# Optimization experiments

Measured on AMD Instinct MI355X. Metric: run time of the kernel, lower is better.

## Reference

```python
import jax, jax.numpy as jnp
from jax import lax
import numpy as np

B, L1, L2 = 64, 1024, 1024


def setup_inputs() -> dict:
    key = jax.random.key(0)
    ks = jax.random.split(key, 6)
    s1 = 1.0 / np.sqrt(L1)
    s2 = 1.0 / np.sqrt(L2)
    return {
        "a": jax.random.normal(ks[0], (B, L1), dtype=jnp.float32),
        "b": jax.random.normal(ks[1], (B, L2), dtype=jnp.float32),
        # nn.Linear(L1, L1) and nn.Linear(L2, L2) params (PyTorch default uniform init range)
        "W1": jax.random.uniform(ks[2], (L1, L1), jnp.float32, -s1, s1),
        "b1": jax.random.uniform(ks[3], (L1,), jnp.float32, -s1, s1),
        "W2": jax.random.uniform(ks[4], (L2, L2), jnp.float32, -s2, s2),
        "b2": jax.random.uniform(ks[5], (L2,), jnp.float32, -s2, s2),
    }


def _dtw_cost(cost):
    """DTW accumulated-cost DP for one [N, M] pairwise-cost matrix.

    R[i,j] = cost[i,j] + min(R[i-1,j-1], R[i-1,j], R[i,j-1]).
    The within-row dependency x[j] = c[j] + min(m[j], x[j-1]) is a min-plus
    prefix: x[j] = S[j] + cummin(m - S_{j-1}) with S = cumsum(c), which lets
    each row be computed in parallel (wavefront-equivalent vectorization).
    Returns the scalar DTW distance R[N-1, M-1].
    """
    dt = cost.dtype
    row0 = jnp.cumsum(cost[0])  # R[0, :]

    def step(prev_row, c_row):
        # m[j] = min(R[i-1, j], R[i-1, j-1]);  j=0 has no (i-1, j-1) neighbor
        shifted = jnp.concatenate([jnp.full((1,), jnp.inf, dt), prev_row[:-1]])
        m = jnp.minimum(prev_row, shifted)
        S = jnp.cumsum(c_row)
        S_prev = jnp.concatenate([jnp.zeros((1,), dt), S[:-1]])
        row = S + lax.associative_scan(jnp.minimum, m - S_prev)
        return row, None

    last_row, _ = lax.scan(step, row0, cost[1:])
    return last_row[-1]


def reference(a, b, W1, b1, W2, b2):
    # seq1 / seq2 linear projections over the time axis
    a_p = a @ W1.T + b1  # [B, L1]
    b_p = b @ W2.T + b2  # [B, L2]
    # squared-euclidean pairwise cost (scipy.sqeuclidean on scalar elements)
    cost = (a_p[:, :, None] - b_p[:, None, :]) ** 2  # [B, L1, L2]
    return jax.vmap(_dtw_cost)(cost)  # [B] DTW distances
```

## Files before the change

kernel.cpp:

```cpp
#include <hip/hip_runtime.h>
#include <math.h>


#define L 1024
#define BATCH 64

__global__ __launch_bounds__(256) void proj_kernel(
    const float* __restrict__ a, const float* __restrict__ b,
    const float* __restrict__ W1, const float* __restrict__ b1,
    const float* __restrict__ W2, const float* __restrict__ b2,
    float* __restrict__ ap, float* __restrict__ bp, int KC) {
  int part = blockIdx.x >> 7;
  int sub = blockIdx.x & 127;
  const float* X;
  const float* W;
  const float* bias;
  float* out;
  int i0;
  if (sub < 64) {
    X = a; W = W1; bias = b1; out = ap + part * BATCH * L; i0 = sub * 16;
  } else {
    X = b; W = W2; bias = b2; out = bp + part * BATCH * L; i0 = (sub - 64) * 16;
  }

  __shared__ float a_s[64][36];
  __shared__ float w_s[16][36];

  int tid = threadIdx.x;
  int lane_b = tid & 63;
  int iq = tid >> 6;

  float acc[4] = {0.f, 0.f, 0.f, 0.f};

  int kbeg = part * KC;
  int kend = kbeg + KC;
  for (int k0 = kbeg; k0 < kend; k0 += 32) {
    {
      int row = tid >> 2;
      int kl = (tid & 3) * 8;
      const float4* src = reinterpret_cast<const float4*>(&X[row * L + k0 + kl]);
      float4 v0 = src[0];
      float4 v1 = src[1];
      *reinterpret_cast<float4*>(&a_s[row][kl]) = v0;
      *reinterpret_cast<float4*>(&a_s[row][kl + 4]) = v1;
    }
    {
      int row = tid >> 4;
      int kl = (tid & 15) * 2;
      float2 v = *reinterpret_cast<const float2*>(&W[(i0 + row) * L + k0 + kl]);
      w_s[row][kl] = v.x;
      w_s[row][kl + 1] = v.y;
    }
    __syncthreads();
    #pragma unroll
    for (int kl = 0; kl < 32; kl += 4) {
      float4 av = *reinterpret_cast<const float4*>(&a_s[lane_b][kl]);
      #pragma unroll
      for (int m = 0; m < 4; ++m) {
        float4 wv = *reinterpret_cast<const float4*>(&w_s[iq * 4 + m][kl]);
        acc[m] += av.x * wv.x + av.y * wv.y + av.z * wv.z + av.w * wv.w;
      }
    }
    __syncthreads();
  }

  #pragma unroll
  for (int m = 0; m < 4; ++m) {
    int i = i0 + iq * 4 + m;
    float bv = (part == 0) ? bias[i] : 0.f;
    out[lane_b * L + i] = acc[m] + bv;
  }
}


#define NW 4
#define CPL 4
#define KBAR 32
#define OFF 31
#define NG 67
#define APOFF 864
#define APPAD 3048

__device__ __forceinline__ float dpp_shr1_z(float v) {
  int r = __builtin_amdgcn_update_dpp(0, __float_as_int(v), 0x138, 0xf, 0xf,
                                      true);
  return __int_as_float(r);
}

__device__ __forceinline__ float dpp_shl1_z(float v) {
  int r = __builtin_amdgcn_update_dpp(0, __float_as_int(v), 0x130, 0xf, 0xf,
                                      true);
  return __int_as_float(r);
}

__device__ __forceinline__ float min3f(float x, float y, float z) {
  float r;
  asm("v_min3_f32 %0, %1, %2, %3" : "=v"(r) : "v"(x), "v"(y), "v"(z));
  return r;
}

__global__ __launch_bounds__(256, 1) void dtw_kernel(
    const float* __restrict__ app, const float* __restrict__ bpp,
    float* __restrict__ out, int parts) {
  const int b = blockIdx.x;
  const int tid = threadIdx.x;
  const int w = tid >> 6;
  const int t = tid & 63;
  const int woff = OFF * w;
  const float INF = INFINITY;

  __shared__ float ap_pad[APPAD];
  __shared__ float ring[NW - 1][64];

  for (int idx = tid; idx < APPAD; idx += 256) {
    int src = idx - APOFF;
    float v = INF;
    if ((unsigned)src < (unsigned)L) {
      v = app[b * L + src];
      for (int p = 1; p < parts; ++p) v += app[p * BATCH * L + b * L + src];
    }
    ap_pad[idx] = v;
  }
  if (tid < (NW - 1) * 64) reinterpret_cast<float*>(ring)[tid] = INF;

  const int colb = tid * CPL;
  float4 bv = *reinterpret_cast<const float4*>(&bpp[b * L + colb]);
  for (int p = 1; p < parts; ++p) {
    float4 u = *reinterpret_cast<const float4*>(
        &bpp[p * BATCH * L + b * L + colb]);
    bv.x += u.x; bv.y += u.y; bv.z += u.z; bv.w += u.w;
  }
  const float bpv0 = bv.x, bpv1 = bv.y, bpv2 = bv.z, bpv3 = bv.w;

  float p1_0 = INF, p1_1 = INF, p1_2 = INF, p1_3 = INF;
  float p2_0 = INF, p2_1 = INF, p2_2 = INF, p2_3 = INF;
  float A0 = INF, A1 = INF, A2 = INF, A3 = INF;
  float ringchunk = INF, feedprev = INF, vprod = INF, apchunk;
  float res = 0.f;
  const bool lane0 = (t == 0);
  const bool lane63 = (t == 63);
  const int apbase = APOFF + t - (256 + OFF) * w;

  __syncthreads();

#define DTW_GROUP(s0v, FIRSTG, LASTG)                                        \
  {                                                                          \
    const int s0 = (s0v);                                                    \
    apchunk = ap_pad[apbase + s0];                                           \
    if (w == 0)                                                              \
      ringchunk = INF;                                                       \
    else if (t < KBAR)                                                       \
      ringchunk = ring[w - 1][(s0 + t - woff - 1) & 63];                     \
    _Pragma("unroll")                                                        \
    for (int k = 0; k < KBAR; ++k) {                                         \
      float sh1 = dpp_shr1_z(p1_3);                                          \
      float sh2 = dpp_shr1_z(p2_3);                                          \
      float sha = dpp_shr1_z(A3);                                            \
      float p1m1 = lane0 ? ringchunk : sh1;                                  \
      float p2m1 = lane0 ? feedprev : sh2;                                   \
      if ((FIRSTG) && k == 0 && w == 0) p2m1 = lane0 ? 0.f : sh2;            \
      feedprev = ringchunk;                                                  \
      ringchunk = dpp_shl1_z(ringchunk);                                     \
      A3 = A2; A2 = A1; A1 = A0;                                             \
      A0 = lane0 ? apchunk : sha;                                            \
      apchunk = dpp_shl1_z(apchunk);                                         \
      float d0 = A0 - bpv0, d1 = A1 - bpv1;                                  \
      float d2 = A2 - bpv2, d3 = A3 - bpv3;                                  \
      float b0 = min3f(p1_0, p1m1, p2m1);                                    \
      float b1 = min3f(p1_1, p1_0, p2_0);                                    \
      float b2 = min3f(p1_2, p1_1, p2_1);                                    \
      float b3 = min3f(p1_3, p1_2, p2_2);                                    \
      float x0 = __builtin_fmaf(d0, d0, b0);                                 \
      float x1 = __builtin_fmaf(d1, d1, b1);                                 \
      float x2 = __builtin_fmaf(d2, d2, b2);                                 \
      float x3 = __builtin_fmaf(d3, d3, b3);                                 \
      p2_0 = p1_0; p2_1 = p1_1; p2_2 = p1_2; p2_3 = p1_3;                    \
      p1_0 = x0; p1_1 = x1; p1_2 = x2; p1_3 = x3;                            \
      vprod = dpp_shl1_z(vprod);                                             \
      vprod = lane63 ? x3 : vprod;                                           \
      if ((LASTG) && k == 27) res = x3;                                      \
    }                                                                        \
    if (w < NW - 1 && t >= 64 - KBAR)                                        \
      ring[w][(s0 + t - 32 - woff) & 63] = vprod;                            \
    __syncthreads();                                                         \
  }

  DTW_GROUP(0, true, false);
  for (int g = 1; g < NG - 1; ++g) DTW_GROUP(g * KBAR, false, false);
  DTW_GROUP((NG - 1) * KBAR, false, true);
#undef DTW_GROUP

  if (w == NW - 1 && t == 63) out[b] = res;
}

extern "C" void kernel_launch(void* const* d_in, const int* in_sizes, int n_in,
                              void* d_out, int out_size, void* d_ws, size_t ws_size,
                              hipStream_t stream) {
  const float* a  = (const float*)d_in[0];
  const float* b  = (const float*)d_in[1];
  const float* W1 = (const float*)d_in[2];
  const float* b1 = (const float*)d_in[3];
  const float* W2 = (const float*)d_in[4];
  const float* b2 = (const float*)d_in[5];
  float* out = (float*)d_out;

  size_t per_part = (size_t)2 * BATCH * L * sizeof(float);
  int parts = 1;
  if (ws_size >= 4 * per_part) parts = 4;
  else if (ws_size >= 2 * per_part) parts = 2;

  float* ap = (float*)d_ws;
  float* bp = ap + (size_t)parts * BATCH * L;

  proj_kernel<<<128 * parts, 256, 0, stream>>>(a, b, W1, b1, W2, b2,
                                               ap, bp, L / parts);
  dtw_kernel<<<BATCH, 256, 0, stream>>>(ap, bp, out, parts);
}
```

Measured before the change: 106.1 us.

## Double DTW wavefronts per block and halve columns per lane

The DTW kernel now uses 8 wavefronts of 512 threads, each lane owning 2 columns instead of 4. This shortens the serial dependency chain per step, since each lane does half the min3/fma work per anti-diagonal. The cost is more pipeline groups (71 vs 67) and more block-wide barriers across more waves. The p2m1 handling is also simplified by carrying the previous p1m1 instead of tracking a separate feed value.

```diff
diff --git a/kernel.cpp b/kernel.cpp
--- a/kernel.cpp
+++ b/kernel.cpp
@@ -73,13 +73,13 @@
 }
 
 
-#define NW 4
-#define CPL 4
+#define NW 8
+#define CPL 2
 #define KBAR 32
 #define OFF 31
-#define NG 67
-#define APOFF 864
-#define APPAD 3048
+#define NG 71
+#define APOFF 1248
+#define APPAD 3560
 
 __device__ __forceinline__ float dpp_shr1_z(float v) {
   int r = __builtin_amdgcn_update_dpp(0, __float_as_int(v), 0x138, 0xf, 0xf,
@@ -99,7 +99,7 @@
   return r;
 }
 
-__global__ __launch_bounds__(256, 1) void dtw_kernel(
+__global__ __launch_bounds__(512, 1) void dtw_kernel(
     const float* __restrict__ app, const float* __restrict__ bpp,
     float* __restrict__ out, int parts) {
   const int b = blockIdx.x;
@@ -112,7 +112,7 @@
   __shared__ float ap_pad[APPAD];
   __shared__ float ring[NW - 1][64];
 
-  for (int idx = tid; idx < APPAD; idx += 256) {
+  for (int idx = tid; idx < APPAD; idx += 512) {
     int src = idx - APOFF;
     float v = INF;
     if ((unsigned)src < (unsigned)L) {
@@ -124,70 +124,63 @@
   if (tid < (NW - 1) * 64) reinterpret_cast<float*>(ring)[tid] = INF;
 
   const int colb = tid * CPL;
-  float4 bv = *reinterpret_cast<const float4*>(&bpp[b * L + colb]);
+  float2 bv = *reinterpret_cast<const float2*>(&bpp[b * L + colb]);
   for (int p = 1; p < parts; ++p) {
-    float4 u = *reinterpret_cast<const float4*>(
+    float2 u = *reinterpret_cast<const float2*>(
         &bpp[p * BATCH * L + b * L + colb]);
-    bv.x += u.x; bv.y += u.y; bv.z += u.z; bv.w += u.w;
-  }
-  const float bpv0 = bv.x, bpv1 = bv.y, bpv2 = bv.z, bpv3 = bv.w;
-
-  float p1_0 = INF, p1_1 = INF, p1_2 = INF, p1_3 = INF;
-  float p2_0 = INF, p2_1 = INF, p2_2 = INF, p2_3 = INF;
-  float A0 = INF, A1 = INF, A2 = INF, A3 = INF;
-  float ringchunk = INF, feedprev = INF, vprod = INF, apchunk;
+    bv.x += u.x; bv.y += u.y;
+  }
+  const float bpv0 = bv.x, bpv1 = bv.y;
+
+  float p1_0 = INF, p1_1 = INF;
+  float p2_0 = INF;
+  float p2m1c = (w == 0 && t == 0) ? 0.f : INF;
+  float A0 = INF, A1 = INF;
+  float ringchunk = INF, vprod = INF, apchunk;
   float res = 0.f;
   const bool lane0 = (t == 0);
   const bool lane63 = (t == 63);
-  const int apbase = APOFF + t - (256 + OFF) * w;
+  const int apbase = APOFF - (128 + OFF) * w;
 
   __syncthreads();
 
-#define DTW_GROUP(s0v, FIRSTG, LASTG)                                        \
+#define DTW_GROUP(s0v, LASTG)                                                \
   {                                                                          \
     const int s0 = (s0v);                                                    \
-    apchunk = ap_pad[apbase + s0];                                           \
+    apchunk = ap_pad[apbase + s0 + t - 2 * 0];                               \
     if (w == 0)                                                              \
       ringchunk = INF;                                                       \
     else if (t < KBAR)                                                       \
       ringchunk = ring[w - 1][(s0 + t - woff - 1) & 63];                     \
     _Pragma("unroll")                                                        \
     for (int k = 0; k < KBAR; ++k) {                                         \
-      float sh1 = dpp_shr1_z(p1_3);                                          \
-      float sh2 = dpp_shr1_z(p2_3);                                          \
-      float sha = dpp_shr1_z(A3);                                            \
+      float sh1 = dpp_shr1_z(p1_1);                                          \
       float p1m1 = lane0 ? ringchunk : sh1;                                  \
-      float p2m1 = lane0 ? feedprev : sh2;                                   \
-      if ((FIRSTG) && k == 0 && w == 0) p2m1 = lane0 ? 0.f : sh2;            \
-      feedprev = ringchunk;                                                  \
       ringchunk = dpp_shl1_z(ringchunk);                                     \
-      A3 = A2; A2 = A1; A1 = A0;                                             \
+      float sha = dpp_shr1_z(A1);                                            \
+      A1 = A0;                                                               \
       A0 = lane0 ? apchunk : sha;                                            \
       apchunk = dpp_shl1_z(apchunk);                                         \
       float d0 = A0 - bpv0, d1 = A1 - bpv1;                                  \
-      float d2 = A2 - bpv2, d3 = A3 - bpv3;                                  \
-      float b0 = min3f(p1_0, p1m1, p2m1);                                    \
+      float b0 = min3f(p1_0, p1m1, p2m1c);                                   \
       float b1 = min3f(p1_1, p1_0, p2_0);                                    \
-      float b2 = min3f(p1_2, p1_1, p2_1);                                    \
-      float b3 = min3f(p1_3, p1_2, p2_2);                                    \
       float x0 = __builtin_fmaf(d0, d0, b0);                                 \
       float x1 = __builtin_fmaf(d1, d1, b1);                                 \
-      float x2 = __builtin_fmaf(d2, d2, b2);                                 \
-      float x3 = __builtin_fmaf(d3, d3, b3);                                 \
-      p2_0 = p1_0; p2_1 = p1_1; p2_2 = p1_2; p2_3 = p1_3;                    \
-      p1_0 = x0; p1_1 = x1; p1_2 = x2; p1_3 = x3;                            \
+      p2m1c = p1m1;                                                          \
+      p2_0 = p1_0;                                                           \
+      p1_0 = x0;                                                             \
+      p1_1 = x1;                                                             \
       vprod = dpp_shl1_z(vprod);                                             \
-      vprod = lane63 ? x3 : vprod;                                           \
-      if ((LASTG) && k == 27) res = x3;                                      \
+      vprod = lane63 ? x1 : vprod;                                           \
+      if ((LASTG) && k == 23) res = x1;                                      \
     }                                                                        \
     if (w < NW - 1 && t >= 64 - KBAR)                                        \
       ring[w][(s0 + t - 32 - woff) & 63] = vprod;                            \
     __syncthreads();                                                         \
   }
 
-  DTW_GROUP(0, true, false);
-  for (int g = 1; g < NG - 1; ++g) DTW_GROUP(g * KBAR, false, false);
-  DTW_GROUP((NG - 1) * KBAR, false, true);
+  for (int g = 0; g < NG - 1; ++g) DTW_GROUP(g * KBAR, false);
+  DTW_GROUP((NG - 1) * KBAR, true);
 #undef DTW_GROUP
 
   if (w == NW - 1 && t == 63) out[b] = res;
@@ -214,5 +207,5 @@
 
   proj_kernel<<<128 * parts, 256, 0, stream>>>(a, b, W1, b1, W2, b2,
                                                ap, bp, L / parts);
-  dtw_kernel<<<BATCH, 256, 0, stream>>>(ap, bp, out, parts);
-}
+  dtw_kernel<<<BATCH, 512, 0, stream>>>(ap, bp, out, parts);
+}
```

Measured after the change: 139.7 us. 1.32x slower.
